# Performance work log

Hardware: AMD Instinct MI355X
Metric: run time of the kernel (lower is better)

Reference implementation:

```python
import jax, jax.numpy as jnp
import numpy as np

NUM_ROUNDS = 2
NUM_REVERSE_ROUNDS = 2


def _scatter_mean(x, src, dst, n):
    # PyG mean aggregation: out[i] = mean_{(src->i) in E} x[src]; 0 if no in-edges.
    deg = jax.ops.segment_sum(jnp.ones((src.shape[0],), x.dtype), dst, num_segments=n)
    s = jax.ops.segment_sum(x[src], dst, num_segments=n)
    return s / jnp.maximum(deg, 1.0)[:, None]


def setup_inputs() -> dict:
    key = jax.random.key(0)
    ks = jax.random.split(key, 12)
    N_TEXT, N_NON, E, EMB, R = 100000, 10000, 500000, 256, 500
    N = N_TEXT + N_NON
    PRED_IN = 4 * EMB + 2 * 2 + 2 * 2 * (NUM_ROUNDS + NUM_REVERSE_ROUNDS)  # 1044
    return {
        "h_id_tensor": jax.random.randint(ks[0], (E,), 0, N),
        "r_id_tensor": jax.random.randint(ks[1], (E,), 0, R),
        "t_id_tensor": jax.random.randint(ks[2], (E,), 0, N),
        "q_emb": jax.random.normal(ks[3], (EMB,), jnp.float32),
        "entity_embs": jax.random.normal(ks[4], (N_TEXT, EMB), jnp.float32),
        "num_non_text_entities": N_NON,
        "relation_embs": jax.random.normal(ks[5], (R, EMB), jnp.float32),
        "topic_entity_one_hot": jax.random.uniform(ks[6], (N, 2), jnp.float32),
        "non_text_emb": jax.random.normal(ks[7], (1, EMB), jnp.float32),
        "W1": jax.random.normal(ks[8], (PRED_IN, EMB), jnp.float32) * 0.02,
        "b1": jnp.zeros((EMB,), jnp.float32),
        "W2": jax.random.normal(ks[9], (EMB, 1), jnp.float32) * 0.02,
        "b2": jnp.zeros((1,), jnp.float32),
    }


def reference(h_id_tensor, r_id_tensor, t_id_tensor, q_emb, entity_embs,
              num_non_text_entities, relation_embs, topic_entity_one_hot,
              non_text_emb, W1, b1, W2, b2):
    n = entity_embs.shape[0] + num_non_text_entities
    # h_e base: text entity embs + broadcast non-text embedding
    h_e0 = jnp.concatenate(
        [entity_embs, jnp.broadcast_to(non_text_emb, (num_non_text_entities, non_text_emb.shape[1]))],
        axis=0)
    h_e_list = [h_e0, topic_entity_one_hot]
    # DDE forward rounds: messages flow h_id -> t_id
    h_pe = topic_entity_one_hot
    for _ in range(NUM_ROUNDS):
        h_pe = _scatter_mean(h_pe, h_id_tensor, t_id_tensor, n)
        h_e_list.append(h_pe)
    # reverse rounds: messages flow t_id -> h_id
    h_pe = topic_entity_one_hot
    for _ in range(NUM_REVERSE_ROUNDS):
        h_pe = _scatter_mean(h_pe, t_id_tensor, h_id_tensor, n)
        h_e_list.append(h_pe)
    h_e = jnp.concatenate(h_e_list, axis=1)  # [N, emb + 2 + 2*(R+Rr)]
    e = h_id_tensor.shape[0]
    h_triple = jnp.concatenate(
        [jnp.broadcast_to(q_emb[None, :], (e, q_emb.shape[0])),
         h_e[h_id_tensor],
         relation_embs[r_id_tensor],
         h_e[t_id_tensor]], axis=1)  # [E, 1044]
    hidden = jax.nn.relu(h_triple @ W1 + b1)
    return hidden @ W2 + b2
```

## Files before the change

kernel.cpp:

```cpp
#include <hip/hip_runtime.h>
#include <stdint.h>

#define EMB 256
#define LDK 288
#define DDE 10

typedef __attribute__((ext_vector_type(8))) short short8;
typedef __attribute__((ext_vector_type(4))) float f32x4;
typedef __attribute__((ext_vector_type(4))) int int4v;

__device__ __forceinline__ unsigned short f2bf(float f) {
    union { float f; unsigned int u; } v; v.f = f;
    unsigned int u = v.u;
    unsigned int r = (u + 0x7FFFu + ((u >> 16) & 1u)) >> 16;
    return (unsigned short)r;
}
__device__ __forceinline__ float bf2f(unsigned short b) {
    union { unsigned int u; float f; } v; v.u = ((unsigned int)b) << 16;
    return v.f;
}

#define FPSCALE 1048576.0f
#define FPINV   (1.0f / 1048576.0f)

__device__ __forceinline__ unsigned long long pack2(float a, float b) {
    unsigned int ua = (unsigned int)(a * FPSCALE);
    unsigned int ub = (unsigned int)(b * FPSCALE);
    return ((unsigned long long)ua << 36) | ((unsigned long long)ub << 10);
}
__device__ __forceinline__ float2 unpack2(unsigned long long v) {
    float d = fmaxf((float)(unsigned int)(v & 0x3FFULL), 1.0f);
    return make_float2((float)((v >> 36) & 0x3FFFFFFULL) * FPINV / d,
                       (float)((v >> 10) & 0x3FFFFFFULL) * FPINV / d);
}
__device__ __forceinline__ float2 unpack2d(unsigned long long v, float d) {
    return make_float2((float)((v >> 36) & 0x3FFFFFFULL) * FPINV / d,
                       (float)((v >> 10) & 0x3FFFFFFULL) * FPINV / d);
}


__global__ void k_r1_fused(const int* __restrict__ h_id, const int* __restrict__ t_id,
                           const float2* __restrict__ topic,
                           unsigned long long* __restrict__ fwd,
                           unsigned long long* __restrict__ rev, int E, int SC1, int COPY, int WT_BLK,
                           int TOTAL,
                           const float4* __restrict__ entity, const float4* __restrict__ nontext,
                           ushort4* __restrict__ he4, int n_text, int N,
                           const float* __restrict__ W1, unsigned short* __restrict__ wT,
                           const float* __restrict__ qv, const float* __restrict__ rel,
                           const float* __restrict__ b1, unsigned short* __restrict__ Prb) {
    const int b = blockIdx.x;
    const int sc_before = (int)(((long long)b * SC1) / TOTAL);
    const int is_scatter = (int)(((long long)(b + 1) * SC1) / TOTAL) != sc_before;
    if (is_scatter) {
        int e = sc_before * 256 + threadIdx.x;
        if (e >= E) return;
        int h = h_id[e], t = t_id[e];
        float2 th = topic[h];
        float2 tt = topic[t];
        atomicAdd(&fwd[t], pack2(th.x, th.y) | 1ULL);
        atomicAdd(&rev[h], pack2(tt.x, tt.y) | 1ULL);
        return;
    }
    const int o = b - sc_before;
    if (o < COPY) {
        int idx = o * 256 + threadIdx.x;
        int n = idx >> 6, q = idx & 63;
        float4 v = make_float4(0.f, 0.f, 0.f, 0.f);
        if (n < N) v = (n < n_text) ? entity[(size_t)n * 64 + q] : nontext[q];
        he4[(size_t)n * (LDK / 4) + q] = make_ushort4(f2bf(v.x), f2bf(v.y), f2bf(v.z), f2bf(v.w));
    } else if (o < COPY + WT_BLK) {
        int idx = (o - COPY) * 256 + threadIdx.x;
        int j = idx / LDK;
        int k = idx - j * LDK;
        int col   = (j < EMB) ? j : (j - EMB);
        int baseE = (j < EMB) ? 256 : 778;
        int baseD = (j < EMB) ? 512 : 1034;
        float v = 0.0f;
        if (k < EMB)            v = W1[(long long)(baseE + k) * EMB + col];
        else if (k < EMB + DDE) v = W1[(long long)(baseD + (k - EMB)) * EMB + col];
        wT[idx] = f2bf(v);
    } else {
        int r = o - COPY - WT_BLK;
        int j = threadIdx.x;
        float acc = b1[j];
        for (int k = 0; k < EMB; ++k)
            acc = fmaf(qv[k], W1[(long long)k * EMB + j], acc);
        const float* relr = rel + (long long)r * EMB;
        for (int k = 0; k < EMB; ++k)
            acc = fmaf(relr[k], W1[(long long)(522 + k) * EMB + j], acc);
        Prb[(long long)r * EMB + j] = f2bf(acc);
    }
}


__global__ void k_r2(const int* __restrict__ h_id, const int* __restrict__ t_id,
                     const unsigned long long* __restrict__ fwd,
                     const unsigned long long* __restrict__ rev,
                     unsigned long long* __restrict__ s2,
                     unsigned long long* __restrict__ sr2, int E) {
    int e = blockIdx.x * blockDim.x + threadIdx.x;
    if (e >= E) return;
    int h = h_id[e], t = t_id[e];
    float2 dh = unpack2(fwd[h]);
    float2 rt = unpack2(rev[t]);
    atomicAdd(&s2[t], pack2(dh.x, dh.y));
    atomicAdd(&sr2[h], pack2(rt.x, rt.y));
}


__global__ void k_tail(const float2* __restrict__ topic,
                       const unsigned long long* __restrict__ fwd,
                       const unsigned long long* __restrict__ rev,
                       const unsigned long long* __restrict__ s2,
                       const unsigned long long* __restrict__ sr2,
                       ushort4* __restrict__ he4, int N, int Mpad) {
    int idx = blockIdx.x * blockDim.x + threadIdx.x;
    if (idx >= Mpad * 8) return;
    int n = idx >> 3, j = idx & 7;
    float4 v = make_float4(0.f, 0.f, 0.f, 0.f);
    if (n < N && j < 3) {
        if (j == 0) {
            float2 a = topic[n];
            float2 b = unpack2(fwd[n]);
            v = make_float4(a.x, a.y, b.x, b.y);
        } else if (j == 1) {
            float df = fmaxf((float)(unsigned int)(fwd[n] & 0x3FFULL), 1.0f);
            float2 a = unpack2d(s2[n], df);
            float2 b = unpack2(rev[n]);
            v = make_float4(a.x, a.y, b.x, b.y);
        } else {
            float dr = fmaxf((float)(unsigned int)(rev[n] & 0x3FFULL), 1.0f);
            float2 a = unpack2d(sr2[n], dr);
            v = make_float4(a.x, a.y, 0.f, 0.f);
        }
    }
    he4[(size_t)n * (LDK / 4) + 64 + j] = make_ushort4(f2bf(v.x), f2bf(v.y), f2bf(v.z), f2bf(v.w));
}

__global__ __launch_bounds__(512) void k_gemm(const unsigned short* __restrict__ he,
                                              const unsigned short* __restrict__ wT,
                                              unsigned short* __restrict__ Ph,
                                              unsigned short* __restrict__ Pt) {
    __shared__ __align__(16) unsigned short lA[128 * 32];
    __shared__ __align__(16) unsigned short lB[256 * 32];
    const int t = threadIdx.x;
    const int lane = t & 63;
    const int w = t >> 6;
    const int bswz = (blockIdx.x & 7) * ((int)gridDim.x >> 3) + (blockIdx.x >> 3);
    const int br = bswz >> 1;
    const int bc = bswz & 1;
    const int wr = w >> 2;
    const int wc = w & 3;

    f32x4 acc[4][4];
#pragma unroll
    for (int r = 0; r < 4; ++r)
#pragma unroll
        for (int c = 0; c < 4; ++c)
            acc[r][c] = (f32x4){0.f, 0.f, 0.f, 0.f};

    const char* baseA = (const char*)he + (size_t)(br * 128) * (LDK * 2);
    const char* baseB = (const char*)wT + (size_t)(bc * 256) * (LDK * 2);

    const int rowX = t >> 2;
    const int colb = (t & 3) * 16;

    for (int k0 = 0; k0 < LDK; k0 += 32) {
        __syncthreads();
        {
            const char* srcA  = baseA + (size_t)rowX * (LDK * 2) + k0 * 2 + colb;
            const char* srcB0 = baseB + (size_t)rowX * (LDK * 2) + k0 * 2 + colb;
            const char* srcB1 = baseB + (size_t)(rowX + 128) * (LDK * 2) + k0 * 2 + colb;
            __builtin_amdgcn_global_load_lds((const __attribute__((address_space(1))) void*)srcA,
                                             (__attribute__((address_space(3))) void*)((char*)lA + t * 16), 16, 0, 0);
            __builtin_amdgcn_global_load_lds((const __attribute__((address_space(1))) void*)srcB0,
                                             (__attribute__((address_space(3))) void*)((char*)lB + t * 16), 16, 0, 0);
            __builtin_amdgcn_global_load_lds((const __attribute__((address_space(1))) void*)srcB1,
                                             (__attribute__((address_space(3))) void*)((char*)lB + 8192 + t * 16), 16, 0, 0);
        }
        __syncthreads();

        short8 af[4], bfr[4];
#pragma unroll
        for (int r = 0; r < 4; ++r) {
            int arow = wr * 64 + r * 16 + (lane & 15);
            af[r] = *(const short8*)(lA + arow * 32 + (lane >> 4) * 8);
        }
#pragma unroll
        for (int c = 0; c < 4; ++c) {
            int brow = wc * 64 + c * 16 + (lane & 15);
            bfr[c] = *(const short8*)(lB + brow * 32 + (lane >> 4) * 8);
        }
#pragma unroll
        for (int r = 0; r < 4; ++r)
#pragma unroll
            for (int c = 0; c < 4; ++c)
                acc[r][c] = __builtin_amdgcn_mfma_f32_16x16x32_bf16(af[r], bfr[c], acc[r][c], 0, 0, 0);
    }

    unsigned short* Pout = bc ? Pt : Ph;
    const int nbase = wc * 64;
    const int mbase = br * 128 + wr * 64 + (lane >> 4) * 4;
#pragma unroll
    for (int r = 0; r < 4; ++r) {
#pragma unroll
        for (int c = 0; c < 4; ++c) {
            int n = nbase + c * 16 + (lane & 15);
#pragma unroll
            for (int i = 0; i < 4; ++i) {
                int m = mbase + r * 16 + i;
                Pout[(size_t)m * EMB + n] = f2bf(acc[r][c][i]);
            }
        }
    }
}

__device__ __forceinline__ short8 ntload(const unsigned short* p) {
    union { int4v i; short8 s; } u;
    u.i = __builtin_nontemporal_load((const int4v*)p);
    return u.s;
}

__global__ __launch_bounds__(256) void k_edge(
    const int* __restrict__ h_id, const int* __restrict__ r_id, const int* __restrict__ t_id,
    const unsigned short* __restrict__ Ph, const unsigned short* __restrict__ Pt,
    const unsigned short* __restrict__ Prb, const float* __restrict__ W2,
    const float* __restrict__ b2, float* __restrict__ out, int E) {
    const int lane = threadIdx.x & 63;
    const int half = lane >> 5;
    const int l32  = lane & 31;
    const int gw = (blockIdx.x * blockDim.x + threadIdx.x) >> 6;
    const int nw = (gridDim.x * blockDim.x) >> 6;
    const int lo = l32 * 8;
    float w2v[8];
    *(float4*)&w2v[0] = *(const float4*)(W2 + lo);
    *(float4*)&w2v[4] = *(const float4*)(W2 + lo + 4);
    const float bb = b2[0];

    for (int e0 = gw * 4; e0 < E; e0 += nw * 4) {
        short8 ph[2], pt[2], pr[2];
        int ev[2];
#pragma unroll
        for (int p = 0; p < 2; ++p) {
            int e = e0 + 2 * p + half;
            ev[p] = e;
            int ec = (e < E) ? e : 0;
            int h = h_id[ec], r = r_id[ec], t = t_id[ec];
            ph[p] = ntload(Ph + (size_t)h * EMB + lo);
            pt[p] = ntload(Pt + (size_t)t * EMB + lo);
            pr[p] = *(const short8*)(Prb + (size_t)r * EMB + lo);
        }
#pragma unroll
        for (int p = 0; p < 2; ++p) {
            float acc = 0.f;
#pragma unroll
            for (int j = 0; j < 8; ++j) {
                float v = bf2f((unsigned short)pr[p][j]) + bf2f((unsigned short)ph[p][j])
                        + bf2f((unsigned short)pt[p][j]);
                acc += fmaxf(v, 0.f) * w2v[j];
            }
#pragma unroll
            for (int m = 16; m >= 1; m >>= 1) acc += __shfl_xor(acc, m, 64);
            if (l32 == 0 && ev[p] < E) out[ev[p]] = acc + bb;
        }
    }
}


extern "C" void kernel_launch(void* const* d_in, const int* in_sizes, int n_in,
                              void* d_out, int out_size, void* d_ws, size_t ws_size,
                              hipStream_t stream) {
    const int*   h_id    = (const int*)d_in[0];
    const int*   r_id    = (const int*)d_in[1];
    const int*   t_id    = (const int*)d_in[2];
    const float* q       = (const float*)d_in[3];
    const float* entity  = (const float*)d_in[4];
    const float* rel     = (const float*)d_in[6];
    const float* topic   = (const float*)d_in[7];
    const float* nontext = (const float*)d_in[8];
    const float* W1      = (const float*)d_in[9];
    const float* b1      = (const float*)d_in[10];
    const float* W2      = (const float*)d_in[11];
    const float* b2      = (const float*)d_in[12];

    const int E      = in_sizes[0];
    const int n_text = in_sizes[4] / EMB;
    const int N      = in_sizes[7] / 2;
    const int R      = in_sizes[6] / EMB;
    const int Mpad   = (N + 127) & ~127;

    char* p = (char*)d_ws;
    auto alloc = [&](size_t bytes) {
        char* r = p;
        p += (bytes + 255) & ~(size_t)255;
        return r;
    };
    unsigned long long* fwd = (unsigned long long*)alloc((size_t)Mpad * 8);
    unsigned long long* rev = (unsigned long long*)alloc((size_t)Mpad * 8);
    unsigned long long* s2  = (unsigned long long*)alloc((size_t)Mpad * 8);
    unsigned long long* sr2 = (unsigned long long*)alloc((size_t)Mpad * 8);
    size_t zero_bytes = (size_t)(p - (char*)d_ws);
    unsigned short* he  = (unsigned short*)alloc((size_t)Mpad * LDK * 2);
    unsigned short* wT  = (unsigned short*)alloc((size_t)512 * LDK * 2);
    unsigned short* Prb = (unsigned short*)alloc((size_t)R * EMB * 2);
    unsigned short* Ph  = (unsigned short*)alloc((size_t)Mpad * EMB * 2);
    unsigned short* Pt  = (unsigned short*)alloc((size_t)Mpad * EMB * 2);

    hipMemsetAsync(d_ws, 0, zero_bytes, stream);

    const int T = 256;
    const int SC1 = (E + T - 1) / T;
    const int COPY = Mpad / 4;
    const int WT_BLK = (512 * LDK) / T;
    const int TOTAL = SC1 + COPY + WT_BLK + R;

    k_r1_fused<<<TOTAL, T, 0, stream>>>(
        h_id, t_id, (const float2*)topic, fwd, rev, E, SC1, COPY, WT_BLK, TOTAL,
        (const float4*)entity, (const float4*)nontext, (ushort4*)he, n_text, N,
        W1, wT, q, rel, b1, Prb);
    k_r2<<<SC1, T, 0, stream>>>(h_id, t_id, fwd, rev, s2, sr2, E);
    k_tail<<<(Mpad * 8 + T - 1) / T, T, 0, stream>>>(
        (const float2*)topic, fwd, rev, s2, sr2, (ushort4*)he, N, Mpad);

    k_gemm<<<(Mpad / 128) * 2, 512, 0, stream>>>(he, wT, Ph, Pt);

    k_edge<<<4096, T, 0, stream>>>(h_id, r_id, t_id, Ph, Pt, Prb, W2, b2, (float*)d_out, E);
}
```

Before: 312.9 us.

## Fuse DDE tail features into GEMM A-tile load and simplify edge kernel

Removes the k_tail kernel. The GEMM now builds the final 32-wide K slab of the A tile in LDS directly from topic/fwd/rev/s2/sr2, so he is stored with a 256-wide stride instead of 288. The edge kernel is also rewritten to handle one edge per wavefront with ushort4 loads and a 64-lane reduction, dropping the non-temporal loads and the 2-edge batching, and its grid is doubled. This saves one launch and the 288-wide he writes and reads, but the edge kernel gets less memory-level parallelism per wave.

```diff
diff --git a/kernel.cpp b/kernel.cpp
--- a/kernel.cpp
+++ b/kernel.cpp
@@ -2,12 +2,11 @@
 #include <stdint.h>
 
 #define EMB 256
-#define LDK 288
+#define LDKB 288
 #define DDE 10
 
 typedef __attribute__((ext_vector_type(8))) short short8;
 typedef __attribute__((ext_vector_type(4))) float f32x4;
-typedef __attribute__((ext_vector_type(4))) int int4v;
 
 __device__ __forceinline__ unsigned short f2bf(float f) {
     union { float f; unsigned int u; } v; v.f = f;
@@ -68,11 +67,11 @@
         int n = idx >> 6, q = idx & 63;
         float4 v = make_float4(0.f, 0.f, 0.f, 0.f);
         if (n < N) v = (n < n_text) ? entity[(size_t)n * 64 + q] : nontext[q];
-        he4[(size_t)n * (LDK / 4) + q] = make_ushort4(f2bf(v.x), f2bf(v.y), f2bf(v.z), f2bf(v.w));
+        he4[(size_t)n * 64 + q] = make_ushort4(f2bf(v.x), f2bf(v.y), f2bf(v.z), f2bf(v.w));
     } else if (o < COPY + WT_BLK) {
         int idx = (o - COPY) * 256 + threadIdx.x;
-        int j = idx / LDK;
-        int k = idx - j * LDK;
+        int j = idx / LDKB;
+        int k = idx - j * LDKB;
         int col   = (j < EMB) ? j : (j - EMB);
         int baseE = (j < EMB) ? 256 : 778;
         int baseD = (j < EMB) ? 512 : 1034;
@@ -108,40 +107,16 @@
     atomicAdd(&sr2[h], pack2(rt.x, rt.y));
 }
 
-
-__global__ void k_tail(const float2* __restrict__ topic,
-                       const unsigned long long* __restrict__ fwd,
-                       const unsigned long long* __restrict__ rev,
-                       const unsigned long long* __restrict__ s2,
-                       const unsigned long long* __restrict__ sr2,
-                       ushort4* __restrict__ he4, int N, int Mpad) {
-    int idx = blockIdx.x * blockDim.x + threadIdx.x;
-    if (idx >= Mpad * 8) return;
-    int n = idx >> 3, j = idx & 7;
-    float4 v = make_float4(0.f, 0.f, 0.f, 0.f);
-    if (n < N && j < 3) {
-        if (j == 0) {
-            float2 a = topic[n];
-            float2 b = unpack2(fwd[n]);
-            v = make_float4(a.x, a.y, b.x, b.y);
-        } else if (j == 1) {
-            float df = fmaxf((float)(unsigned int)(fwd[n] & 0x3FFULL), 1.0f);
-            float2 a = unpack2d(s2[n], df);
-            float2 b = unpack2(rev[n]);
-            v = make_float4(a.x, a.y, b.x, b.y);
-        } else {
-            float dr = fmaxf((float)(unsigned int)(rev[n] & 0x3FFULL), 1.0f);
-            float2 a = unpack2d(sr2[n], dr);
-            v = make_float4(a.x, a.y, 0.f, 0.f);
-        }
-    }
-    he4[(size_t)n * (LDK / 4) + 64 + j] = make_ushort4(f2bf(v.x), f2bf(v.y), f2bf(v.z), f2bf(v.w));
-}
-
 __global__ __launch_bounds__(512) void k_gemm(const unsigned short* __restrict__ he,
                                               const unsigned short* __restrict__ wT,
                                               unsigned short* __restrict__ Ph,
-                                              unsigned short* __restrict__ Pt) {
+                                              unsigned short* __restrict__ Pt,
+                                              const float2* __restrict__ topic,
+                                              const unsigned long long* __restrict__ fwd,
+                                              const unsigned long long* __restrict__ rev,
+                                              const unsigned long long* __restrict__ s2,
+                                              const unsigned long long* __restrict__ sr2,
+                                              int N) {
     __shared__ __align__(16) unsigned short lA[128 * 32];
     __shared__ __align__(16) unsigned short lB[256 * 32];
     const int t = threadIdx.x;
@@ -160,20 +135,47 @@
         for (int c = 0; c < 4; ++c)
             acc[r][c] = (f32x4){0.f, 0.f, 0.f, 0.f};
 
-    const char* baseA = (const char*)he + (size_t)(br * 128) * (LDK * 2);
-    const char* baseB = (const char*)wT + (size_t)(bc * 256) * (LDK * 2);
+    const char* baseA = (const char*)he + (size_t)(br * 128) * (EMB * 2);
+    const char* baseB = (const char*)wT + (size_t)(bc * 256) * (LDKB * 2);
 
     const int rowX = t >> 2;
     const int colb = (t & 3) * 16;
 
-    for (int k0 = 0; k0 < LDK; k0 += 32) {
+    for (int k0 = 0; k0 < LDKB; k0 += 32) {
         __syncthreads();
-        {
-            const char* srcA  = baseA + (size_t)rowX * (LDK * 2) + k0 * 2 + colb;
-            const char* srcB0 = baseB + (size_t)rowX * (LDK * 2) + k0 * 2 + colb;
-            const char* srcB1 = baseB + (size_t)(rowX + 128) * (LDK * 2) + k0 * 2 + colb;
+        if (k0 < EMB) {
+            const char* srcA = baseA + (size_t)rowX * (EMB * 2) + k0 * 2 + colb;
             __builtin_amdgcn_global_load_lds((const __attribute__((address_space(1))) void*)srcA,
                                              (__attribute__((address_space(3))) void*)((char*)lA + t * 16), 16, 0, 0);
+        } else {
+            const int n = br * 128 + rowX;
+            short8 hv = (short8){0, 0, 0, 0, 0, 0, 0, 0};
+            const int q4 = t & 3;
+            if (n < N) {
+                if (q4 == 0) {
+                    float2 tp = topic[n];
+                    unsigned long long f = fwd[n];
+                    unsigned long long r = rev[n];
+                    float df = fmaxf((float)(unsigned int)(f & 0x3FFULL), 1.0f);
+                    float2 d1 = unpack2d(f, df);
+                    float2 d2 = unpack2d(s2[n], df);
+                    float2 r1 = unpack2(r);
+                    hv[0] = (short)f2bf(tp.x); hv[1] = (short)f2bf(tp.y);
+                    hv[2] = (short)f2bf(d1.x); hv[3] = (short)f2bf(d1.y);
+                    hv[4] = (short)f2bf(d2.x); hv[5] = (short)f2bf(d2.y);
+                    hv[6] = (short)f2bf(r1.x); hv[7] = (short)f2bf(r1.y);
+                } else if (q4 == 1) {
+                    unsigned long long r = rev[n];
+                    float dr = fmaxf((float)(unsigned int)(r & 0x3FFULL), 1.0f);
+                    float2 r2 = unpack2d(sr2[n], dr);
+                    hv[0] = (short)f2bf(r2.x); hv[1] = (short)f2bf(r2.y);
+                }
+            }
+            *(short8*)((char*)lA + rowX * 64 + q4 * 16) = hv;
+        }
+        {
+            const char* srcB0 = baseB + (size_t)rowX * (LDKB * 2) + k0 * 2 + colb;
+            const char* srcB1 = baseB + (size_t)(rowX + 128) * (LDKB * 2) + k0 * 2 + colb;
             __builtin_amdgcn_global_load_lds((const __attribute__((address_space(1))) void*)srcB0,
                                              (__attribute__((address_space(3))) void*)((char*)lB + t * 16), 16, 0, 0);
             __builtin_amdgcn_global_load_lds((const __attribute__((address_space(1))) void*)srcB1,
@@ -214,12 +216,6 @@
             }
         }
     }
-}
-
-__device__ __forceinline__ short8 ntload(const unsigned short* p) {
-    union { int4v i; short8 s; } u;
-    u.i = __builtin_nontemporal_load((const int4v*)p);
-    return u.s;
 }
 
 __global__ __launch_bounds__(256) void k_edge(
@@ -227,43 +223,25 @@
     const unsigned short* __restrict__ Ph, const unsigned short* __restrict__ Pt,
     const unsigned short* __restrict__ Prb, const float* __restrict__ W2,
     const float* __restrict__ b2, float* __restrict__ out, int E) {
-    const int lane = threadIdx.x & 63;
-    const int half = lane >> 5;
-    const int l32  = lane & 31;
-    const int gw = (blockIdx.x * blockDim.x + threadIdx.x) >> 6;
-    const int nw = (gridDim.x * blockDim.x) >> 6;
-    const int lo = l32 * 8;
-    float w2v[8];
-    *(float4*)&w2v[0] = *(const float4*)(W2 + lo);
-    *(float4*)&w2v[4] = *(const float4*)(W2 + lo + 4);
-    const float bb = b2[0];
-
-    for (int e0 = gw * 4; e0 < E; e0 += nw * 4) {
-        short8 ph[2], pt[2], pr[2];
-        int ev[2];
-#pragma unroll
-        for (int p = 0; p < 2; ++p) {
-            int e = e0 + 2 * p + half;
-            ev[p] = e;
-            int ec = (e < E) ? e : 0;
-            int h = h_id[ec], r = r_id[ec], t = t_id[ec];
-            ph[p] = ntload(Ph + (size_t)h * EMB + lo);
-            pt[p] = ntload(Pt + (size_t)t * EMB + lo);
-            pr[p] = *(const short8*)(Prb + (size_t)r * EMB + lo);
-        }
-#pragma unroll
-        for (int p = 0; p < 2; ++p) {
-            float acc = 0.f;
-#pragma unroll
-            for (int j = 0; j < 8; ++j) {
-                float v = bf2f((unsigned short)pr[p][j]) + bf2f((unsigned short)ph[p][j])
-                        + bf2f((unsigned short)pt[p][j]);
-                acc += fmaxf(v, 0.f) * w2v[j];
-            }
-#pragma unroll
-            for (int m = 16; m >= 1; m >>= 1) acc += __shfl_xor(acc, m, 64);
-            if (l32 == 0 && ev[p] < E) out[ev[p]] = acc + bb;
-        }
+    int lane = threadIdx.x & 63;
+    int gw = (blockIdx.x * blockDim.x + threadIdx.x) >> 6;
+    int nw = (gridDim.x * blockDim.x) >> 6;
+    float4 w2 = *(const float4*)(W2 + 4 * lane);
+    float bb = b2[0];
+    const int lo = 4 * lane;
+    for (int e = gw; e < E; e += nw) {
+        int h = h_id[e], r = r_id[e], t = t_id[e];
+        ushort4 ph = *(const ushort4*)(Ph + (size_t)h * EMB + lo);
+        ushort4 pt = *(const ushort4*)(Pt + (size_t)t * EMB + lo);
+        ushort4 pr = *(const ushort4*)(Prb + (size_t)r * EMB + lo);
+        float v, acc;
+        v = bf2f(pr.x) + bf2f(ph.x) + bf2f(pt.x); acc  = fmaxf(v, 0.f) * w2.x;
+        v = bf2f(pr.y) + bf2f(ph.y) + bf2f(pt.y); acc += fmaxf(v, 0.f) * w2.y;
+        v = bf2f(pr.z) + bf2f(ph.z) + bf2f(pt.z); acc += fmaxf(v, 0.f) * w2.z;
+        v = bf2f(pr.w) + bf2f(ph.w) + bf2f(pt.w); acc += fmaxf(v, 0.f) * w2.w;
+#pragma unroll
+        for (int m = 32; m >= 1; m >>= 1) acc += __shfl_xor(acc, m, 64);
+        if (lane == 0) out[e] = acc + bb;
     }
 }
 
@@ -301,8 +279,8 @@
     unsigned long long* s2  = (unsigned long long*)alloc((size_t)Mpad * 8);
     unsigned long long* sr2 = (unsigned long long*)alloc((size_t)Mpad * 8);
     size_t zero_bytes = (size_t)(p - (char*)d_ws);
-    unsigned short* he  = (unsigned short*)alloc((size_t)Mpad * LDK * 2);
-    unsigned short* wT  = (unsigned short*)alloc((size_t)512 * LDK * 2);
+    unsigned short* he  = (unsigned short*)alloc((size_t)Mpad * EMB * 2);
+    unsigned short* wT  = (unsigned short*)alloc((size_t)512 * LDKB * 2);
     unsigned short* Prb = (unsigned short*)alloc((size_t)R * EMB * 2);
     unsigned short* Ph  = (unsigned short*)alloc((size_t)Mpad * EMB * 2);
     unsigned short* Pt  = (unsigned short*)alloc((size_t)Mpad * EMB * 2);
@@ -312,7 +290,7 @@
     const int T = 256;
     const int SC1 = (E + T - 1) / T;
     const int COPY = Mpad / 4;
-    const int WT_BLK = (512 * LDK) / T;
+    const int WT_BLK = (512 * LDKB) / T;
     const int TOTAL = SC1 + COPY + WT_BLK + R;
 
     k_r1_fused<<<TOTAL, T, 0, stream>>>(
@@ -320,10 +298,9 @@
         (const float4*)entity, (const float4*)nontext, (ushort4*)he, n_text, N,
         W1, wT, q, rel, b1, Prb);
     k_r2<<<SC1, T, 0, stream>>>(h_id, t_id, fwd, rev, s2, sr2, E);
-    k_tail<<<(Mpad * 8 + T - 1) / T, T, 0, stream>>>(
-        (const float2*)topic, fwd, rev, s2, sr2, (ushort4*)he, N, Mpad);
-
-    k_gemm<<<(Mpad / 128) * 2, 512, 0, stream>>>(he, wT, Ph, Pt);
-
-    k_edge<<<4096, T, 0, stream>>>(h_id, r_id, t_id, Ph, Pt, Prb, W2, b2, (float*)d_out, E);
-}
+
+    k_gemm<<<(Mpad / 128) * 2, 512, 0, stream>>>(he, wT, Ph, Pt,
+                                                 (const float2*)topic, fwd, rev, s2, sr2, N);
+
+    k_edge<<<8192, T, 0, stream>>>(h_id, r_id, t_id, Ph, Pt, Prb, W2, b2, (float*)d_out, E);
+}
```

Result: faster. 304.6 us (-2.6%).
